# Optimization experiments

Measured on AMD Instinct MI355X. Metric: run time of the kernel, lower is better.

The kernel has to match this reference:

```python
import jax, jax.numpy as jnp
import numpy as np

EPSILON = 0.05
MAX_ITER = 30
MAX_TOKENS = 256

def _l2norm(x):
    n = jnp.sqrt(jnp.sum(x * x, axis=-1, keepdims=True))
    return x / jnp.maximum(n, 1e-12)

def _sample_tokens(tokens):
    # tokens: [N, C]; deterministic linspace subsample to MAX_TOKENS (N > MAX_TOKENS here)
    n = tokens.shape[0]
    idx = jnp.linspace(0.0, n - 1.0, MAX_TOKENS).astype(jnp.int32)  # truncation like .long()
    return tokens[idx]

def _sinkhorn_distance(pred_tokens, target_tokens):
    # pred_tokens: [Tp, C], target_tokens: [Tt, C]
    p = _l2norm(pred_tokens)
    t = _l2norm(target_tokens)
    cost = 1.0 - p @ t.T                       # [Tp, Tt]
    log_kernel = -cost / EPSILON
    tp = p.shape[0]
    tt = t.shape[0]
    log_mu = jnp.full((tp,), -np.log(tp), dtype=p.dtype)
    log_nu = jnp.full((tt,), -np.log(tt), dtype=p.dtype)

    def body(_, uv):
        u, v = uv
        u = log_mu - jax.nn.logsumexp(log_kernel + v[None, :], axis=1)
        v = log_nu - jax.nn.logsumexp(log_kernel + u[:, None], axis=0)
        return (u, v)

    u0 = jnp.zeros((tp,), dtype=p.dtype)
    v0 = jnp.zeros((tt,), dtype=p.dtype)
    u, v = jax.lax.fori_loop(0, MAX_ITER, body, (u0, v0))
    transport = jnp.exp(log_kernel + u[:, None] + v[None, :])
    return jnp.sum(transport * cost)

def setup_inputs() -> dict:
    key = jax.random.key(0)
    k1, k2 = jax.random.split(key)
    B, C, H, W = 64, 256, 64, 64
    pred_feature = jax.random.normal(k1, (B, C, H, W), dtype=jnp.float32)
    target_feature = jax.random.normal(k2, (B, C, H, W), dtype=jnp.float32)
    return {"pred_feature": pred_feature, "target_feature": target_feature}

def reference(pred_feature, target_feature):
    B, C, H, W = pred_feature.shape
    # (B,C,H,W) -> (B, H*W, C), then deterministic token subsampling to MAX_TOKENS
    pt = pred_feature.transpose(0, 2, 3, 1).reshape(B, H * W, C)
    tt = target_feature.transpose(0, 2, 3, 1).reshape(B, H * W, C)
    pt = jax.vmap(_sample_tokens)(pt)   # [B, MAX_TOKENS, C]
    tt = jax.vmap(_sample_tokens)(tt)
    losses = jax.vmap(_sinkhorn_distance)(pt, tt)  # [B]
    return jnp.mean(losses)
```

## Files before the change

kernel.cpp:

```cpp
#include <hip/hip_runtime.h>

#define BATCH 64
#define CH    256
#define HW    4096
#define TOK   256
#define ITERS 30

constexpr float K2SCALE   = 28.853900817779268f;
constexpr float LOSSSCALE = -0.034657359027997264f;

#define TOKP_OFF 0
#define TOKT_OFF (BATCH*CH*TOK)
#define K2_OFF   (2*BATCH*CH*TOK)
#define LOSS_OFF (K2_OFF + BATCH*TOK*TOK)

__device__ __forceinline__ float fexp2(float x) {
#if __has_builtin(__builtin_amdgcn_exp2f)
    return __builtin_amdgcn_exp2f(x);
#else
    return exp2f(x);
#endif
}
__device__ __forceinline__ float flog2(float x) {
#if __has_builtin(__builtin_amdgcn_logf)
    return __builtin_amdgcn_logf(x);
#else
    return log2f(x);
#endif
}

__device__ __forceinline__ int sample_pos(int i) {
    const float step = 4095.0f / 255.0f;
    return (int)((float)i * step);
}

__global__ __launch_bounds__(256) void gather_kernel(
        const float* __restrict__ pred, const float* __restrict__ targ,
        float* __restrict__ ws) {
    int bx = blockIdx.x;
    int b  = bx >> 6;
    int t  = (bx >> 5) & 1;
    int ch = bx & 31;
    int i  = threadIdx.x;
    int pos = sample_pos(i);

    const float* src = (t ? targ : pred)
                     + (size_t)b * CH * HW + (size_t)(ch * 8) * HW + pos;
    float* dst = ws + (t ? TOKT_OFF : TOKP_OFF)
                    + (size_t)b * CH * TOK + (size_t)(ch * 8) * TOK + i;

    float v[8];
#pragma unroll
    for (int cc = 0; cc < 8; ++cc) v[cc] = src[(size_t)cc * HW];
#pragma unroll
    for (int cc = 0; cc < 8; ++cc) dst[(size_t)cc * TOK] = v[cc];
}

__global__ __launch_bounds__(256) void gemm_kernel(float* __restrict__ ws) {
    __shared__ float at[32][132];
    __shared__ float bt[32][132];
    __shared__ float rnA[128];
    __shared__ float rnB[128];

    int bx = blockIdx.x;
    int b = bx >> 2, tile = bx & 3;
    int i0 = (tile >> 1) * 128;
    int j0 = (tile & 1) * 128;
    int tid = threadIdx.x;
    int tx = tid & 15, ty = tid >> 4;

    const float* tp = ws + TOKP_OFF + (size_t)b * CH * TOK;
    const float* tt = ws + TOKT_OFF + (size_t)b * CH * TOK;

    float acc[8][8] = {};
    float sa = 0.0f, sb = 0.0f;

    for (int chnk = 0; chnk < 8; ++chnk) {
#pragma unroll
        for (int q = 0; q < 16; ++q) {
            int idx = q * 256 + tid;
            int cc = idx >> 7, col = idx & 127;
            float va = tp[(size_t)(chnk * 32 + cc) * TOK + i0 + col];
            float vb = tt[(size_t)(chnk * 32 + cc) * TOK + j0 + col];
            at[cc][col] = va;
            bt[cc][col] = vb;
            sa = fmaf(va, va, sa);
            sb = fmaf(vb, vb, sb);
        }
        __syncthreads();
#pragma unroll
        for (int cc = 0; cc < 32; ++cc) {
            float4 a0 = *(const float4*)&at[cc][tx * 4];
            float4 a1 = *(const float4*)&at[cc][64 + tx * 4];
            float4 b0 = *(const float4*)&bt[cc][ty * 4];
            float4 b1 = *(const float4*)&bt[cc][64 + ty * 4];
            float af[8] = {a0.x, a0.y, a0.z, a0.w, a1.x, a1.y, a1.z, a1.w};
            float bf[8] = {b0.x, b0.y, b0.z, b0.w, b1.x, b1.y, b1.z, b1.w};
#pragma unroll
            for (int r = 0; r < 8; ++r)
#pragma unroll
                for (int c = 0; c < 8; ++c)
                    acc[r][c] = fmaf(af[r], bf[c], acc[r][c]);
        }
        __syncthreads();
    }

    if (tid >= 128) { rnA[tid - 128] = sa; rnB[tid - 128] = sb; }
    __syncthreads();
    if (tid < 128) {
        float fa = sa + rnA[tid];
        float fb = sb + rnB[tid];
        rnA[tid] = 1.0f / fmaxf(sqrtf(fa), 1e-12f);
        rnB[tid] = 1.0f / fmaxf(sqrtf(fb), 1e-12f);
    }
    __syncthreads();

    float rpf[8], rtf[8];
#pragma unroll
    for (int r = 0; r < 8; ++r) rpf[r] = rnA[4 * tx + (r & 3) + 64 * (r >> 2)];
#pragma unroll
    for (int c = 0; c < 8; ++c) rtf[c] = rnB[4 * ty + (c & 3) + 64 * (c >> 2)];

    float* K2w = ws + K2_OFF + (size_t)b * TOK * TOK;
#pragma unroll
    for (int r = 0; r < 8; ++r) {
        float out[8];
#pragma unroll
        for (int c = 0; c < 8; ++c)
            out[c] = (acc[r][c] * rpf[r] * rtf[c] - 1.0f) * K2SCALE;
        size_t row = (size_t)(i0 + 4 * tx + (r & 3) + 64 * (r >> 2)) * TOK;
        *(float4*)&K2w[row + j0 + 4 * ty]      = make_float4(out[0], out[1], out[2], out[3]);
        *(float4*)&K2w[row + j0 + 64 + 4 * ty] = make_float4(out[4], out[5], out[6], out[7]);
    }
}

__global__ __launch_bounds__(1024, 1) void sinkhorn_kernel(float* __restrict__ ws) {
    __shared__ float red[256][33];
    __shared__ float wuperm[256];
    __shared__ float wvperm[256];
    __shared__ float wsum[16];

    int b = blockIdx.x;
    int tid = threadIdx.x;
    int ti = tid >> 5, tj = tid & 31;

    const float* K2r = ws + K2_OFF + (size_t)b * TOK * TOK;
    float e[8][8];
#pragma unroll
    for (int r = 0; r < 8; ++r) {
        const float4* p = (const float4*)&K2r[(size_t)(8 * ti + r) * TOK + 8 * tj];
        float4 v0 = p[0], v1 = p[1];
        e[r][0] = fexp2(v0.x); e[r][1] = fexp2(v0.y);
        e[r][2] = fexp2(v0.z); e[r][3] = fexp2(v0.w);
        e[r][4] = fexp2(v1.x); e[r][5] = fexp2(v1.y);
        e[r][6] = fexp2(v1.z); e[r][7] = fexp2(v1.w);
    }

    if (tid < 256) wvperm[tid] = 1.0f;
    __syncthreads();

    for (int it = 0; it < ITERS; ++it) {
        float wv[8];
#pragma unroll
        for (int c = 0; c < 8; ++c) wv[c] = wvperm[tj + 32 * c];
#pragma unroll
        for (int r = 0; r < 8; ++r) {
            float s = 0.0f;
#pragma unroll
            for (int c = 0; c < 8; ++c) s = fmaf(e[r][c], wv[c], s);
            red[ti + 32 * r][tj] = s;
        }
        __syncthreads();
        if (tid < 256) {
            float s = 0.0f;
#pragma unroll
            for (int q = 0; q < 32; ++q) s += red[tid][q];
            wuperm[tid] = 0.00390625f / s;
        }
        __syncthreads();

        float wu[8];
#pragma unroll
        for (int r = 0; r < 8; ++r) wu[r] = wuperm[ti + 32 * r];
#pragma unroll
        for (int c = 0; c < 8; ++c) {
            float s = 0.0f;
#pragma unroll
            for (int r = 0; r < 8; ++r) s = fmaf(e[r][c], wu[r], s);
            red[tj + 32 * c][ti] = s;
        }
        __syncthreads();
        if (tid < 256) {
            float s = 0.0f;
#pragma unroll
            for (int q = 0; q < 32; ++q) s += red[tid][q];
            wvperm[tid] = 0.00390625f / s;
        }
        __syncthreads();
    }

    float wu[8], wv[8];
#pragma unroll
    for (int r = 0; r < 8; ++r) wu[r] = wuperm[ti + 32 * r];
#pragma unroll
    for (int c = 0; c < 8; ++c) wv[c] = wvperm[tj + 32 * c];

    float acc = 0.0f;
#pragma unroll
    for (int r = 0; r < 8; ++r)
#pragma unroll
        for (int c = 0; c < 8; ++c)
            acc += e[r][c] * wu[r] * wv[c] * flog2(e[r][c]);

#pragma unroll
    for (int off = 32; off >= 1; off >>= 1) acc += __shfl_xor(acc, off, 64);
    int wid = tid >> 6, lane = tid & 63;
    if (lane == 0) wsum[wid] = acc;
    __syncthreads();
    if (tid == 0) {
        float s = 0.0f;
#pragma unroll
        for (int w = 0; w < 16; ++w) s += wsum[w];
        ws[LOSS_OFF + b] = s * LOSSSCALE;
    }
}

__global__ __launch_bounds__(64) void final_kernel(const float* __restrict__ ws,
                                                   float* __restrict__ out) {
    int tid = threadIdx.x;
    float v = ws[LOSS_OFF + tid];
#pragma unroll
    for (int off = 32; off >= 1; off >>= 1) v += __shfl_xor(v, off, 64);
    if (tid == 0) out[0] = v * (1.0f / 64.0f);
}

extern "C" void kernel_launch(void* const* d_in, const int* in_sizes, int n_in,
                              void* d_out, int out_size, void* d_ws, size_t ws_size,
                              hipStream_t stream) {
    const float* pred = (const float*)d_in[0];
    const float* targ = (const float*)d_in[1];
    float* ws = (float*)d_ws;
    float* out = (float*)d_out;

    hipLaunchKernelGGL(gather_kernel,   dim3(4096), dim3(256),  0, stream, pred, targ, ws);
    hipLaunchKernelGGL(gemm_kernel,     dim3(256),  dim3(256),  0, stream, ws);
    hipLaunchKernelGGL(sinkhorn_kernel, dim3(64),   dim3(1024), 0, stream, ws);
    hipLaunchKernelGGL(final_kernel,    dim3(1),    dim3(64),   0, stream, ws, out);
}
```

Before: 603.0 us.

## Stream full rows through LDS for coalesced gather; shrink GEMM tiles to 128x64

The gather kernel now has each block read whole 4096-float channel rows with coalesced float4 loads into shared memory, then pick the 256 sampled positions from LDS. Before, each thread read a single strided element. This targets the scattered per-element global loads, since the sample stride roughly touches every cache line anyway. The cost is extra LDS traffic and two barriers per row. The GEMM kernel also moves from 128x128 to 128x64 output tiles, doubling the grid to 512 blocks and allowing 2 blocks per CU, so more CUs have work. The price is less operand reuse per block and a more involved norm reduction for the B tile.

```diff
diff --git a/kernel.cpp b/kernel.cpp
--- a/kernel.cpp
+++ b/kernel.cpp
@@ -37,42 +37,54 @@
 __global__ __launch_bounds__(256) void gather_kernel(
         const float* __restrict__ pred, const float* __restrict__ targ,
         float* __restrict__ ws) {
+    __shared__ float lds[HW];
+    int i   = threadIdx.x;
+    int pos = sample_pos(i);
+    int p0  = blockIdx.x * 8;
+
+    for (int q = 0; q < 8; ++q) {
+        int p   = p0 + q;
+        int b   = p >> 9;
+        int rem = p & 511;
+        int t   = rem >> 8;
+        int c   = rem & 255;
+
+        const float4* src4 = (const float4*)((t ? targ : pred)
+                              + ((size_t)b * CH + c) * HW);
+        float4 v0 = src4[i];
+        float4 v1 = src4[i + 256];
+        float4 v2 = src4[i + 512];
+        float4 v3 = src4[i + 768];
+        float4* l4 = (float4*)lds;
+        l4[i]       = v0;
+        l4[i + 256] = v1;
+        l4[i + 512] = v2;
+        l4[i + 768] = v3;
+        __syncthreads();
+        float val = lds[pos];
+        ws[(t ? TOKT_OFF : TOKP_OFF) + ((size_t)b * CH + c) * TOK + i] = val;
+        __syncthreads();
+    }
+}
+
+__global__ __launch_bounds__(256, 2) void gemm_kernel(float* __restrict__ ws) {
+    __shared__ float at[32][132];
+    __shared__ float bt[32][68];
+    __shared__ float rnA[128];
+    __shared__ float rnB4[3][64];
+    __shared__ float rnB[64];
+
     int bx = blockIdx.x;
-    int b  = bx >> 6;
-    int t  = (bx >> 5) & 1;
-    int ch = bx & 31;
-    int i  = threadIdx.x;
-    int pos = sample_pos(i);
-
-    const float* src = (t ? targ : pred)
-                     + (size_t)b * CH * HW + (size_t)(ch * 8) * HW + pos;
-    float* dst = ws + (t ? TOKT_OFF : TOKP_OFF)
-                    + (size_t)b * CH * TOK + (size_t)(ch * 8) * TOK + i;
-
-    float v[8];
-#pragma unroll
-    for (int cc = 0; cc < 8; ++cc) v[cc] = src[(size_t)cc * HW];
-#pragma unroll
-    for (int cc = 0; cc < 8; ++cc) dst[(size_t)cc * TOK] = v[cc];
-}
-
-__global__ __launch_bounds__(256) void gemm_kernel(float* __restrict__ ws) {
-    __shared__ float at[32][132];
-    __shared__ float bt[32][132];
-    __shared__ float rnA[128];
-    __shared__ float rnB[128];
-
-    int bx = blockIdx.x;
-    int b = bx >> 2, tile = bx & 3;
-    int i0 = (tile >> 1) * 128;
-    int j0 = (tile & 1) * 128;
+    int b = bx >> 3, tile = bx & 7;
+    int i0 = (tile >> 2) * 128;
+    int j0 = (tile & 3) * 64;
     int tid = threadIdx.x;
     int tx = tid & 15, ty = tid >> 4;
 
     const float* tp = ws + TOKP_OFF + (size_t)b * CH * TOK;
     const float* tt = ws + TOKT_OFF + (size_t)b * CH * TOK;
 
-    float acc[8][8] = {};
+    float acc[8][4] = {};
     float sa = 0.0f, sb = 0.0f;
 
     for (int chnk = 0; chnk < 8; ++chnk) {
@@ -81,10 +93,15 @@
             int idx = q * 256 + tid;
             int cc = idx >> 7, col = idx & 127;
             float va = tp[(size_t)(chnk * 32 + cc) * TOK + i0 + col];
+            at[cc][col] = va;
+            sa = fmaf(va, va, sa);
+        }
+#pragma unroll
+        for (int q = 0; q < 8; ++q) {
+            int idx = q * 256 + tid;
+            int cc = idx >> 6, col = idx & 63;
             float vb = tt[(size_t)(chnk * 32 + cc) * TOK + j0 + col];
-            at[cc][col] = va;
             bt[cc][col] = vb;
-            sa = fmaf(va, va, sa);
             sb = fmaf(vb, vb, sb);
         }
         __syncthreads();
@@ -93,44 +110,45 @@
             float4 a0 = *(const float4*)&at[cc][tx * 4];
             float4 a1 = *(const float4*)&at[cc][64 + tx * 4];
             float4 b0 = *(const float4*)&bt[cc][ty * 4];
-            float4 b1 = *(const float4*)&bt[cc][64 + ty * 4];
             float af[8] = {a0.x, a0.y, a0.z, a0.w, a1.x, a1.y, a1.z, a1.w};
-            float bf[8] = {b0.x, b0.y, b0.z, b0.w, b1.x, b1.y, b1.z, b1.w};
+            float bf[4] = {b0.x, b0.y, b0.z, b0.w};
 #pragma unroll
             for (int r = 0; r < 8; ++r)
 #pragma unroll
-                for (int c = 0; c < 8; ++c)
+                for (int c = 0; c < 4; ++c)
                     acc[r][c] = fmaf(af[r], bf[c], acc[r][c]);
         }
         __syncthreads();
     }
 
-    if (tid >= 128) { rnA[tid - 128] = sa; rnB[tid - 128] = sb; }
+    if (tid >= 128) rnA[tid - 128] = sa;
+    if (tid >= 64)  rnB4[(tid >> 6) - 1][tid & 63] = sb;
     __syncthreads();
     if (tid < 128) {
         float fa = sa + rnA[tid];
-        float fb = sb + rnB[tid];
         rnA[tid] = 1.0f / fmaxf(sqrtf(fa), 1e-12f);
+    }
+    if (tid < 64) {
+        float fb = sb + rnB4[0][tid] + rnB4[1][tid] + rnB4[2][tid];
         rnB[tid] = 1.0f / fmaxf(sqrtf(fb), 1e-12f);
     }
     __syncthreads();
 
-    float rpf[8], rtf[8];
+    float rpf[8], rtf[4];
 #pragma unroll
     for (int r = 0; r < 8; ++r) rpf[r] = rnA[4 * tx + (r & 3) + 64 * (r >> 2)];
 #pragma unroll
-    for (int c = 0; c < 8; ++c) rtf[c] = rnB[4 * ty + (c & 3) + 64 * (c >> 2)];
+    for (int c = 0; c < 4; ++c) rtf[c] = rnB[4 * ty + c];
 
     float* K2w = ws + K2_OFF + (size_t)b * TOK * TOK;
 #pragma unroll
     for (int r = 0; r < 8; ++r) {
-        float out[8];
-#pragma unroll
-        for (int c = 0; c < 8; ++c)
+        float out[4];
+#pragma unroll
+        for (int c = 0; c < 4; ++c)
             out[c] = (acc[r][c] * rpf[r] * rtf[c] - 1.0f) * K2SCALE;
         size_t row = (size_t)(i0 + 4 * tx + (r & 3) + 64 * (r >> 2)) * TOK;
-        *(float4*)&K2w[row + j0 + 4 * ty]      = make_float4(out[0], out[1], out[2], out[3]);
-        *(float4*)&K2w[row + j0 + 64 + 4 * ty] = make_float4(out[4], out[5], out[6], out[7]);
+        *(float4*)&K2w[row + j0 + 4 * ty] = make_float4(out[0], out[1], out[2], out[3]);
     }
 }
 
@@ -243,7 +261,7 @@
     float* out = (float*)d_out;
 
     hipLaunchKernelGGL(gather_kernel,   dim3(4096), dim3(256),  0, stream, pred, targ, ws);
-    hipLaunchKernelGGL(gemm_kernel,     dim3(256),  dim3(256),  0, stream, ws);
+    hipLaunchKernelGGL(gemm_kernel,     dim3(512),  dim3(256),  0, stream, ws);
     hipLaunchKernelGGL(sinkhorn_kernel, dim3(64),   dim3(1024), 0, stream, ws);
     hipLaunchKernelGGL(final_kernel,    dim3(1),    dim3(64),   0, stream, ws, out);
 }
```

Result: no change. 609.6 us (+1.1%).
